# Kernel optimization log

Hardware: AMD Instinct MI355X
Metric: run time of the kernel (lower is better)

Reference implementation:

```python
import jax, jax.numpy as jnp
import numpy as np

D_MODEL = 2048
NHEAD = 32
GROUPS = 8
HEAD_DIM = D_MODEL // NHEAD  # 64
HPG = NHEAD // GROUPS        # heads per group = 4
ROPE_BASE = 10000.0


def _rope(x):
    # x: [B, H, S, D] -- rotate-half RoPE over full head dim, matching RoPE module
    S, D = x.shape[2], x.shape[3]
    theta = 1.0 / (ROPE_BASE ** (jnp.arange(0, D, 2, dtype=jnp.float32) / D))  # [D/2]
    idx_theta = jnp.arange(S, dtype=jnp.float32)[:, None] * theta[None, :]     # [S, D/2]
    ang = jnp.concatenate([idx_theta, idx_theta], axis=-1)                     # [S, D]
    cos = jnp.cos(ang)[None, None]  # [1,1,S,D]
    sin = jnp.sin(ang)[None, None]
    d2 = D // 2
    neg_half = jnp.concatenate([-x[..., d2:], x[..., :d2]], axis=-1)
    return x * cos + neg_half * sin


def setup_inputs() -> dict:
    key = jax.random.key(0)
    ks = jax.random.split(key, 9)
    B, S = 2, 2048
    s_in = 1.0 / np.sqrt(D_MODEL)
    return {
        "x": jax.random.normal(ks[0], (B, S, D_MODEL), jnp.float32),
        "Wq": jax.random.normal(ks[1], (D_MODEL, D_MODEL), jnp.float32) * s_in,
        "bq": jax.random.normal(ks[2], (D_MODEL,), jnp.float32) * 0.01,
        "Wk": jax.random.normal(ks[3], (HEAD_DIM * GROUPS, D_MODEL), jnp.float32) * s_in,
        "bk": jax.random.normal(ks[4], (HEAD_DIM * GROUPS,), jnp.float32) * 0.01,
        "Wv": jax.random.normal(ks[5], (HEAD_DIM * GROUPS, D_MODEL), jnp.float32) * s_in,
        "bv": jax.random.normal(ks[6], (HEAD_DIM * GROUPS,), jnp.float32) * 0.01,
        "Wo": jax.random.normal(ks[7], (D_MODEL, D_MODEL), jnp.float32) * s_in,
        "bo": jax.random.normal(ks[8], (D_MODEL,), jnp.float32) * 0.01,
    }


def reference(x, Wq, bq, Wk, bk, Wv, bv, Wo, bo):
    B, S, _ = x.shape
    # projections (torch Linear: x @ W.T + b)
    q = (x @ Wq.T + bq).reshape(B, S, NHEAD, HEAD_DIM).transpose(0, 2, 1, 3)   # [B,H,S,D]
    k = (x @ Wk.T + bk).reshape(B, S, GROUPS, HEAD_DIM).transpose(0, 2, 1, 3)  # [B,G,S,D]
    v = (x @ Wv.T + bv).reshape(B, S, GROUPS, HEAD_DIM).transpose(0, 2, 1, 3)  # [B,G,S,D]
    q = _rope(q)
    k = _rope(k)
    # grouped-query attention: share each k/v group across HPG query heads
    qg = q.reshape(B, GROUPS, HPG, S, HEAD_DIM)
    scale = 1.0 / np.sqrt(HEAD_DIM)
    scores = jnp.einsum('bghsd,bgtd->bghst', qg, k) * scale  # [B,G,Hpg,S,S]
    causal = jnp.tril(jnp.ones((S, S), dtype=bool))
    scores = jnp.where(causal, scores, jnp.finfo(scores.dtype).min)
    attn = jax.nn.softmax(scores, axis=-1)
    out = jnp.einsum('bghst,bgtd->bghsd', attn, v)           # [B,G,Hpg,S,D]
    out = out.reshape(B, NHEAD, S, HEAD_DIM).transpose(0, 2, 1, 3).reshape(B, S, D_MODEL)
    return out @ Wo.T + bo
```

## Files before the change

kernel.cpp:

```cpp
#include <hip/hip_runtime.h>

typedef unsigned short u16;
typedef __bf16 bf16x8 __attribute__((ext_vector_type(8)));
typedef float floatx4 __attribute__((ext_vector_type(4)));
typedef u16 u16x8 __attribute__((ext_vector_type(8)));
typedef u16 u16x4 __attribute__((ext_vector_type(4)));

#define D_MODEL 2048
#define S_LEN   2048
#define BATCH   2
#define NHEAD   32
#define GROUPS  8
#define HEAD_DIM 64
#define KV_DIM  512
#define KV_LD   1024

__device__ __forceinline__ float bf2f(u16 h) {
  unsigned int u = ((unsigned int)h) << 16;
  return __builtin_bit_cast(float, u);
}
__device__ __forceinline__ u16 f2bf(float f) {
  unsigned int u = __builtin_bit_cast(unsigned int, f);
  u += 0x7fffu + ((u >> 16) & 1u);
  return (u16)(u >> 16);
}
__device__ __forceinline__ float fexp2(float x) {
  float r;
  asm("v_exp_f32 %0, %1" : "=v"(r) : "v"(x));
  return r;
}

#define GLD_LDS(gp, lp) \
  __builtin_amdgcn_global_load_lds((__attribute__((address_space(1))) void*)(gp), \
                                   (__attribute__((address_space(3))) void*)(lp), 16, 0, 0)

__global__ __launch_bounds__(256)
void cvt5_f32_bf16(const float* s0, const float* s1, const float* s2,
                   const float* s3, const float* s4,
                   u16* d0, u16* d1, u16* d2, u16* d3, u16* d4,
                   int n0, int n1, int n2, int n3, int n4)
{
  const float* s; u16* d; int n;
  switch (blockIdx.y) {
    case 0: s = s0; d = d0; n = n0; break;
    case 1: s = s1; d = d1; n = n1; break;
    case 2: s = s2; d = d2; n = n2; break;
    case 3: s = s3; d = d3; n = n3; break;
    default: s = s4; d = d4; n = n4; break;
  }
  long i = ((long)blockIdx.x * 256 + threadIdx.x) * 8;
  if (i >= n) return;
  floatx4 a = *(const floatx4*)(s + i);
  floatx4 b = *(const floatx4*)(s + i + 4);
  u16x8 r;
#pragma unroll
  for (int j = 0; j < 4; ++j) { r[j] = f2bf(a[j]); r[4 + j] = f2bf(b[j]); }
  *(u16x8*)(d + i) = r;
}

template<bool C_F32>
__global__ __launch_bounds__(256, 3)
void gemm_bt_bias(const u16* __restrict__ A, const u16* __restrict__ W,
                  const float* __restrict__ bias, void* __restrict__ Cv,
                  int K, int ldc)
{
  __shared__ __align__(16) u16 As[128 * 32];
  __shared__ __align__(16) u16 Bs[128 * 32];
  const int t = threadIdx.x;
  const int w = t >> 6, l = t & 63;
  const int lr = l & 15, lq = l >> 4;
  const int wm = (w >> 1) * 64, wn = (w & 1) * 64;
  const long bm = (long)blockIdx.x * 128;
  const long bn = (long)blockIdx.y * 128;

  floatx4 acc[4][4] = {};

  const u16* a0 = A + (bm + (t >> 2)) * (long)K + (t & 3) * 8;
  const u16* a1 = a0 + 64L * K;
  const u16* pB0 = W + (bn + (t >> 2)) * (long)K + (t & 3) * 8;
  const u16* pB1 = pB0 + 64L * K;
  u16* As0 = As + w * 512;
  u16* As1 = As + 2048 + w * 512;
  u16* Bs0 = Bs + w * 512;
  u16* Bs1 = Bs + 2048 + w * 512;

  for (int k0 = 0; k0 < K; k0 += 32) {
    GLD_LDS(a0 + k0, As0);
    GLD_LDS(a1 + k0, As1);
    GLD_LDS(pB0 + k0, Bs0);
    GLD_LDS(pB1 + k0, Bs1);
    __syncthreads();

    bf16x8 av[4], bv[4];
#pragma unroll
    for (int i = 0; i < 4; ++i)
      av[i] = *(const bf16x8*)(As + (wm + i * 16 + lr) * 32 + lq * 8);
#pragma unroll
    for (int j = 0; j < 4; ++j)
      bv[j] = *(const bf16x8*)(Bs + (wn + j * 16 + lr) * 32 + lq * 8);
#pragma unroll
    for (int i = 0; i < 4; ++i)
#pragma unroll
      for (int j = 0; j < 4; ++j)
        acc[i][j] = __builtin_amdgcn_mfma_f32_16x16x32_bf16(av[i], bv[j], acc[i][j], 0, 0, 0);
    __syncthreads();
  }

  float bb[4];
#pragma unroll
  for (int j = 0; j < 4; ++j)
    bb[j] = bias[bn + wn + j * 16 + lr];
#pragma unroll
  for (int i = 0; i < 4; ++i) {
#pragma unroll
    for (int rr = 0; rr < 4; ++rr) {
      long row = bm + wm + i * 16 + lq * 4 + rr;
      long cidx = row * (long)ldc + bn + wn + lr;
#pragma unroll
      for (int j = 0; j < 4; ++j) {
        float v = acc[i][j][rr] + bb[j];
        if (C_F32) ((float*)Cv)[cidx + j * 16] = v;
        else       ((u16*)Cv)[cidx + j * 16] = f2bf(v);
      }
    }
  }
}

__global__ __launch_bounds__(256, 3)
void gemm_bt_bias64(const u16* __restrict__ A, const u16* __restrict__ W,
                    const float* __restrict__ bias0, const float* __restrict__ bias1,
                    u16* __restrict__ C, int K, int ldc, int nsplit)
{
  __shared__ __align__(16) u16 As[64 * 32];
  __shared__ __align__(16) u16 Bs[128 * 32];
  const int t = threadIdx.x;
  const int w = t >> 6, l = t & 63;
  const int lr = l & 15, lq = l >> 4;
  const int wm = (w >> 1) * 32, wn = (w & 1) * 64;
  const long bm = (long)blockIdx.x * 64;
  const long bn = (long)blockIdx.y * 128;

  floatx4 acc[2][4] = {};

  const u16* a0 = A + (bm + (t >> 2)) * (long)K + (t & 3) * 8;
  const u16* pB0 = W + (bn + (t >> 2)) * (long)K + (t & 3) * 8;
  const u16* pB1 = pB0 + 64L * K;
  u16* As0 = As + w * 512;
  u16* Bs0 = Bs + w * 512;
  u16* Bs1 = Bs + 2048 + w * 512;

  for (int k0 = 0; k0 < K; k0 += 32) {
    GLD_LDS(a0 + k0, As0);
    GLD_LDS(pB0 + k0, Bs0);
    GLD_LDS(pB1 + k0, Bs1);
    __syncthreads();

    bf16x8 av[2], bv[4];
#pragma unroll
    for (int i = 0; i < 2; ++i)
      av[i] = *(const bf16x8*)(As + (wm + i * 16 + lr) * 32 + lq * 8);
#pragma unroll
    for (int j = 0; j < 4; ++j)
      bv[j] = *(const bf16x8*)(Bs + (wn + j * 16 + lr) * 32 + lq * 8);
#pragma unroll
    for (int i = 0; i < 2; ++i)
#pragma unroll
      for (int j = 0; j < 4; ++j)
        acc[i][j] = __builtin_amdgcn_mfma_f32_16x16x32_bf16(av[i], bv[j], acc[i][j], 0, 0, 0);
    __syncthreads();
  }

  const float* bias = (bn < nsplit) ? bias0 : (bias1 - nsplit);
  float bb[4];
#pragma unroll
  for (int j = 0; j < 4; ++j)
    bb[j] = bias[bn + wn + j * 16 + lr];
#pragma unroll
  for (int i = 0; i < 2; ++i) {
#pragma unroll
    for (int rr = 0; rr < 4; ++rr) {
      long row = bm + wm + i * 16 + lq * 4 + rr;
      long cidx = row * (long)ldc + bn + wn + lr;
#pragma unroll
      for (int j = 0; j < 4; ++j)
        C[cidx + j * 16] = f2bf(acc[i][j][rr] + bb[j]);
    }
  }
}

__global__ __launch_bounds__(256)
void rope_kernel(u16* __restrict__ Q, u16* __restrict__ KV)
{
  const int bs = blockIdx.x;
  const int s = bs & (S_LEN - 1);
  const int t = threadIdx.x;
  u16* qrow = Q + (long)bs * D_MODEL;
#pragma unroll
  for (int i = 0; i < 4; ++i) {
    int p = t + i * 256;
    int hh = p >> 5, d = p & 31;
    float theta = __expf(-(float)d * 0.28782313662425574f);
    float sn, cs;
    sincosf((float)s * theta, &sn, &cs);
    int i0 = hh * 64 + d;
    float x0 = bf2f(qrow[i0]), x1 = bf2f(qrow[i0 + 32]);
    qrow[i0]      = f2bf(x0 * cs - x1 * sn);
    qrow[i0 + 32] = f2bf(x1 * cs + x0 * sn);
  }
  u16* krow = KV + (long)bs * KV_LD;
  {
    int g = t >> 5, d = t & 31;
    float theta = __expf(-(float)d * 0.28782313662425574f);
    float sn, cs;
    sincosf((float)s * theta, &sn, &cs);
    int i0 = g * 64 + d;
    float x0 = bf2f(krow[i0]), x1 = bf2f(krow[i0 + 32]);
    krow[i0]      = f2bf(x0 * cs - x1 * sn);
    krow[i0 + 32] = f2bf(x1 * cs + x0 * sn);
  }
}

__global__ __launch_bounds__(256)
void vtrans(const u16* __restrict__ KV, u16* __restrict__ Vt)
{
  __shared__ __align__(16) u16 tile[64][72];
  const int ts = blockIdx.x * 64;
  const int tc = blockIdx.y * 64;
  const int b  = blockIdx.z;
  const int t  = threadIdx.x;
#pragma unroll
  for (int i = 0; i < 2; ++i) {
    int c = t + i * 256;
    int r = c >> 3, c8 = (c & 7) * 8;
    u16x8 v = *(const u16x8*)(KV + ((long)b * S_LEN + ts + r) * KV_LD + 512 + tc + c8);
    *(u16x8*)&tile[r][c8] = v;
  }
  __syncthreads();
#pragma unroll
  for (int i = 0; i < 2; ++i) {
    int c = t + i * 256;
    int r = c >> 3, c8 = (c & 7) * 8;
    u16x8 v;
#pragma unroll
    for (int e = 0; e < 8; ++e) v[e] = tile[c8 + e][r];
    *(u16x8*)(Vt + ((long)b * KV_DIM + tc + r) * S_LEN + ts + c8) = v;
  }
}

__global__ __launch_bounds__(256, 3)
void gqa_attn(const u16* Q, const u16* __restrict__ Kc,
              const u16* __restrict__ Vt, u16* O)
{
  __shared__ __align__(16) u16 KV[2][16 * 512];
  __shared__ __align__(16) u16 Ps[4][2][16 * 72];

  const int pr = blockIdx.x;
  const int bh = blockIdx.y;
  const int b = bh >> 5, h = bh & 31, g = h >> 2;

  const int t = threadIdx.x;
  const int w = t >> 6, l = t & 63;
  const int lr = l & 15, lq = l >> 4;

  const u16* Kp = Kc + ((long)b * S_LEN) * KV_LD + g * HEAD_DIM;
  const u16* Vp = Vt + ((long)b * KV_DIM + g * HEAD_DIM) * S_LEN;

  long sb[4];
  {
    const int sig2 = ((l >> 2) ^ (l >> 4)) & 1;
    const int sig1 = ((l >> 1) ^ (l >> 3)) & 1;
    const int sig0 = (l ^ sig2) & 1;
    const int row = ((l >> 2) & 14) | sig2;
    const int cl = ((sig1 << 1) | sig0) * 8;
#pragma unroll
    for (int q = 0; q < 4; ++q) {
      const int r = (w & 1) * 4 + q;
      const int jj = r >> 1, cc = r & 1;
      sb[q] = (w < 2) ? ((long)(jj * 16 + row) * KV_LD + cc * 32 + cl)
                      : ((long)(jj * 16 + row) * S_LEN + cc * 32 + cl);
    }
  }
  const u16* sp = (w < 2) ? Kp : Vp;
  const long smul = (w < 2) ? (long)64 * KV_LD : 64;
  const int dbase = ((w < 2) ? 0 : 4096) + (w & 1) * 2048;
  const int koff = ((4 * lr + lq) ^ (lr & 7)) * 8;

#define STAGE(bufi, kt_) do { \
    const long soff_ = (long)(kt_) * smul; \
    GLD_LDS(sp + soff_ + sb[0], &KV[bufi][dbase + 0 * 512]); \
    GLD_LDS(sp + soff_ + sb[1], &KV[bufi][dbase + 1 * 512]); \
    GLD_LDS(sp + soff_ + sb[2], &KV[bufi][dbase + 2 * 512]); \
    GLD_LDS(sp + soff_ + sb[3], &KV[bufi][dbase + 3 * 512]); \
  } while (0)

#define TILE(ktv, D0, D1) do { \
    const u16* buf_ = &KV[(ktv) & 1][0]; \
    floatx4 z0[4] = {}, z1[4] = {}; \
    _Pragma("unroll") \
    for (int j = 0; j < 4; ++j) { \
      bf16x8 kf0 = *(const bf16x8*)(buf_ + j * 1024 + koff); \
      bf16x8 kf1 = *(const bf16x8*)(buf_ + j * 1024 + 512 + koff); \
      if (!(D1) && (!(D0) || j <= w)) { \
        z0[j] = __builtin_amdgcn_mfma_f32_16x16x32_bf16(kf0, qf00, z0[j], 0, 0, 0); \
        z0[j] = __builtin_amdgcn_mfma_f32_16x16x32_bf16(kf1, qf01, z0[j], 0, 0, 0); \
      } \
      if (!(D1) || j <= w) { \
        z1[j] = __builtin_amdgcn_mfma_f32_16x16x32_bf16(kf0, qf10, z1[j], 0, 0, 0); \
        z1[j] = __builtin_amdgcn_mfma_f32_16x16x32_bf16(kf1, qf11, z1[j], 0, 0, 0); \
      } \
    } \
    if (!(D1)) { \
      _Pragma("unroll") \
      for (int j = 0; j < 4; ++j) { \
        u16x4 pk; \
        _Pragma("unroll") \
        for (int rr = 0; rr < 4; ++rr) { \
          float ps; \
          if ((D0) && (j * 16 + lq * 4 + rr > w * 16 + lr)) ps = 0.f; \
          else ps = fexp2(z0[j][rr] * 0.18033688011112042f - 23.083120654223414f); \
          ls0 += ps; \
          pk[rr] = __builtin_bit_cast(u16, (__bf16)ps); \
        } \
        *(u16x4*)&Ps[w][0][lr * 72 + j * 16 + lq * 4] = pk; \
      } \
    } \
    _Pragma("unroll") \
    for (int j = 0; j < 4; ++j) { \
      u16x4 pk; \
      _Pragma("unroll") \
      for (int rr = 0; rr < 4; ++rr) { \
        float ps; \
        if ((D1) && (j * 16 + lq * 4 + rr > w * 16 + lr)) ps = 0.f; \
        else ps = fexp2(z1[j][rr] * 0.18033688011112042f - 23.083120654223414f); \
        ls1 += ps; \
        pk[rr] = __builtin_bit_cast(u16, (__bf16)ps); \
      } \
      *(u16x4*)&Ps[w][1][lr * 72 + j * 16 + lq * 4] = pk; \
    } \
    bf16x8 pa00 = *(const bf16x8*)&Ps[w][0][lr * 72 + lq * 8]; \
    bf16x8 pa01 = *(const bf16x8*)&Ps[w][0][lr * 72 + 32 + lq * 8]; \
    bf16x8 pa10 = *(const bf16x8*)&Ps[w][1][lr * 72 + lq * 8]; \
    bf16x8 pa11 = *(const bf16x8*)&Ps[w][1][lr * 72 + 32 + lq * 8]; \
    const u16* vbuf_ = buf_ + 4096; \
    _Pragma("unroll") \
    for (int j = 0; j < 4; ++j) { \
      bf16x8 vb0 = *(const bf16x8*)(vbuf_ + j * 1024 + koff); \
      bf16x8 vb1 = *(const bf16x8*)(vbuf_ + j * 1024 + 512 + koff); \
      if (!(D1)) { \
        o0[j] = __builtin_amdgcn_mfma_f32_16x16x32_bf16(pa00, vb0, o0[j], 0, 0, 0); \
        if (!(D0) || w >= 2) \
          o0[j] = __builtin_amdgcn_mfma_f32_16x16x32_bf16(pa01, vb1, o0[j], 0, 0, 0); \
      } \
      o1[j] = __builtin_amdgcn_mfma_f32_16x16x32_bf16(pa10, vb0, o1[j], 0, 0, 0); \
      if (!(D1) || w >= 2) \
        o1[j] = __builtin_amdgcn_mfma_f32_16x16x32_bf16(pa11, vb1, o1[j], 0, 0, 0); \
    } \
  } while (0)

#pragma unroll 1
  for (int seg = 0; seg < 2; ++seg) {
    const int qt = seg ? (15 - pr) : pr;
    const u16* Qp = Q + ((long)b * S_LEN + qt * 128) * D_MODEL + h * HEAD_DIM;
    u16* Op = O + ((long)b * S_LEN + qt * 128) * D_MODEL + h * HEAD_DIM;

    bf16x8 qf00, qf01, qf10, qf11;
    {
      const u16* qr0 = Qp + (long)(w * 16 + lr) * D_MODEL;
      qf00 = *(const bf16x8*)(qr0 + lq * 8);
      qf01 = *(const bf16x8*)(qr0 + 32 + lq * 8);
      const u16* qr1 = qr0 + (long)64 * D_MODEL;
      qf10 = *(const bf16x8*)(qr1 + lq * 8);
      qf11 = *(const bf16x8*)(qr1 + 32 + lq * 8);
    }

    floatx4 o0[4] = {}, o1[4] = {};
    float ls0 = 0.f, ls1 = 0.f;
    const int NKT = 2 * qt + 2;

    if (seg) __syncthreads();
    STAGE(0, 0);
    for (int kt = 0; kt < NKT - 2; ++kt) {
      __syncthreads();
      STAGE((kt + 1) & 1, kt + 1);
      TILE(kt, false, false);
    }
    __syncthreads();
    STAGE((NKT - 1) & 1, NKT - 1);
    TILE(NKT - 2, true, false);
    __syncthreads();
    TILE(NKT - 1, false, true);

#pragma unroll
    for (int s = 0; s < 2; ++s) {
      float ls = s ? ls1 : ls0;
      ls += __shfl_xor(ls, 16);
      ls += __shfl_xor(ls, 32);
      const floatx4* oo = s ? o1 : o0;
#pragma unroll
      for (int rr = 0; rr < 4; ++rr) {
        float lrow = __shfl(ls, lq * 4 + rr);
        float inv = 1.f / lrow;
        long row = s * 64 + w * 16 + lq * 4 + rr;
        u16* op = Op + row * (long)D_MODEL + lr;
#pragma unroll
        for (int j = 0; j < 4; ++j)
          op[j * 16] = f2bf(oo[j][rr] * inv);
      }
    }
  }
#undef TILE
#undef STAGE
}

extern "C" void kernel_launch(void* const* d_in, const int* in_sizes, int n_in,
                              void* d_out, int out_size, void* d_ws, size_t ws_size,
                              hipStream_t stream)
{
  const float* x  = (const float*)d_in[0];
  const float* Wq = (const float*)d_in[1];
  const float* bq = (const float*)d_in[2];
  const float* Wk = (const float*)d_in[3];
  const float* bk = (const float*)d_in[4];
  const float* Wv = (const float*)d_in[5];
  const float* bv = (const float*)d_in[6];
  const float* Wo = (const float*)d_in[7];
  const float* bo = (const float*)d_in[8];
  float* out = (float*)d_out;

  const int Sx  = BATCH * S_LEN * D_MODEL;
  const int SWq = D_MODEL * D_MODEL;
  const int SWk = KV_DIM * D_MODEL;
  const int SWv = KV_DIM * D_MODEL;
  const int SWo = D_MODEL * D_MODEL;

  u16* xb  = (u16*)d_ws;
  u16* Wqb = xb  + Sx;
  u16* Wkb = Wqb + SWq;
  u16* Wvb = Wkb + SWk;
  u16* Wob = Wvb + SWv;
  u16* Qb  = Wob + SWo;
  u16* KVb = Qb + (size_t)4096 * 2048;
  u16* Vtb = KVb + (size_t)4096 * 1024;
  u16* AO  = Qb;

  const int M = BATCH * S_LEN;
  dim3 blk(256);
  cvt5_f32_bf16<<<dim3(4096, 5), blk, 0, stream>>>(x, Wq, Wk, Wv, Wo,
                                                   xb, Wqb, Wkb, Wvb, Wob,
                                                   Sx, SWq, SWk, SWv, SWo);
  gemm_bt_bias<false><<<dim3(M / 128, D_MODEL / 128), blk, 0, stream>>>(xb, Wqb, bq, Qb, D_MODEL, D_MODEL);
  gemm_bt_bias64<<<dim3(M / 64, KV_LD / 128), blk, 0, stream>>>(xb, Wkb, bk, bv, KVb, D_MODEL, KV_LD, KV_DIM);
  vtrans<<<dim3(S_LEN / 64, KV_DIM / 64, BATCH), blk, 0, stream>>>(KVb, Vtb);
  rope_kernel<<<dim3(M), blk, 0, stream>>>(Qb, KVb);
  gqa_attn<<<dim3(8, BATCH * NHEAD), blk, 0, stream>>>(Qb, KVb, Vtb, AO);
  gemm_bt_bias<true><<<dim3(M / 128, D_MODEL / 128), blk, 0, stream>>>(AO, Wob, bo, out, D_MODEL, D_MODEL);
}
```

Measured before the change: 320.9 us.

## Fuse RoPE and V transpose into projection GEMM epilogues with precomputed tables

Builds cos/sin RoPE tables inside the conversion kernel and applies rotation directly in the Q and K GEMM epilogues, where each lane holds both halves of a head. The V projection epilogue writes a transposed V buffer directly. This removes the separate rope and vtrans kernels and their global round trips. K moves to its own compact buffer. The cost is extra table loads in the epilogues and scattered 4-element stores for the transposed V.

```diff
diff --git a/kernel.cpp b/kernel.cpp
--- a/kernel.cpp
+++ b/kernel.cpp
@@ -13,7 +13,6 @@
 #define GROUPS  8
 #define HEAD_DIM 64
 #define KV_DIM  512
-#define KV_LD   1024
 
 __device__ __forceinline__ float bf2f(u16 h) {
   unsigned int u = ((unsigned int)h) << 16;
@@ -38,8 +37,20 @@
 void cvt5_f32_bf16(const float* s0, const float* s1, const float* s2,
                    const float* s3, const float* s4,
                    u16* d0, u16* d1, u16* d2, u16* d3, u16* d4,
-                   int n0, int n1, int n2, int n3, int n4)
+                   int n0, int n1, int n2, int n3, int n4,
+                   float* ct, float* st)
 {
+  if (blockIdx.y == 5) {
+    int idx = blockIdx.x * 256 + threadIdx.x;
+    if (idx < S_LEN * 32) {
+      int s = idx >> 5, d = idx & 31;
+      float theta = __expf(-(float)d * 0.28782313662425574f);
+      float sn, cs;
+      sincosf((float)s * theta, &sn, &cs);
+      ct[idx] = cs; st[idx] = sn;
+    }
+    return;
+  }
   const float* s; u16* d; int n;
   switch (blockIdx.y) {
     case 0: s = s0; d = d0; n = n0; break;
@@ -58,10 +69,11 @@
   *(u16x8*)(d + i) = r;
 }
 
-template<bool C_F32>
+template<int MODE>
 __global__ __launch_bounds__(256, 3)
 void gemm_bt_bias(const u16* __restrict__ A, const u16* __restrict__ W,
                   const float* __restrict__ bias, void* __restrict__ Cv,
+                  const float* __restrict__ ct, const float* __restrict__ st,
                   int K, int ldc)
 {
   __shared__ __align__(16) u16 As[128 * 32];
@@ -110,26 +122,41 @@
 #pragma unroll
   for (int j = 0; j < 4; ++j)
     bb[j] = bias[bn + wn + j * 16 + lr];
+
 #pragma unroll
   for (int i = 0; i < 4; ++i) {
 #pragma unroll
     for (int rr = 0; rr < 4; ++rr) {
       long row = bm + wm + i * 16 + lq * 4 + rr;
       long cidx = row * (long)ldc + bn + wn + lr;
-#pragma unroll
-      for (int j = 0; j < 4; ++j) {
-        float v = acc[i][j][rr] + bb[j];
-        if (C_F32) ((float*)Cv)[cidx + j * 16] = v;
-        else       ((u16*)Cv)[cidx + j * 16] = f2bf(v);
+      if (MODE == 1) {
+        float* cp = (float*)Cv + cidx;
+#pragma unroll
+        for (int j = 0; j < 4; ++j)
+          cp[j * 16] = acc[i][j][rr] + bb[j];
+      } else {
+        int srow = (int)row & (S_LEN - 1);
+        float c0 = ct[srow * 32 + lr],      sn0 = st[srow * 32 + lr];
+        float c1 = ct[srow * 32 + 16 + lr], sn1 = st[srow * 32 + 16 + lr];
+        float v0 = acc[i][0][rr] + bb[0];
+        float v1 = acc[i][1][rr] + bb[1];
+        float v2 = acc[i][2][rr] + bb[2];
+        float v3 = acc[i][3][rr] + bb[3];
+        u16* cp = (u16*)Cv + cidx;
+        cp[0]  = f2bf(v0 * c0 - v2 * sn0);
+        cp[16] = f2bf(v1 * c1 - v3 * sn1);
+        cp[32] = f2bf(v2 * c0 + v0 * sn0);
+        cp[48] = f2bf(v3 * c1 + v1 * sn1);
       }
     }
   }
 }
 
 __global__ __launch_bounds__(256, 3)
-void gemm_bt_bias64(const u16* __restrict__ A, const u16* __restrict__ W,
-                    const float* __restrict__ bias0, const float* __restrict__ bias1,
-                    u16* __restrict__ C, int K, int ldc, int nsplit)
+void gemm_kv(const u16* __restrict__ A, const u16* __restrict__ W,
+             const float* __restrict__ bkb, const float* __restrict__ bvb,
+             u16* __restrict__ Kb, u16* __restrict__ Vt,
+             const float* __restrict__ ct, const float* __restrict__ st, int K)
 {
   __shared__ __align__(16) u16 As[64 * 32];
   __shared__ __align__(16) u16 Bs[128 * 32];
@@ -155,95 +182,64 @@
     GLD_LDS(pB1 + k0, Bs1);
     __syncthreads();
 
-    bf16x8 av[2], bv[4];
+    bf16x8 av[2], bv8[4];
 #pragma unroll
     for (int i = 0; i < 2; ++i)
       av[i] = *(const bf16x8*)(As + (wm + i * 16 + lr) * 32 + lq * 8);
 #pragma unroll
     for (int j = 0; j < 4; ++j)
-      bv[j] = *(const bf16x8*)(Bs + (wn + j * 16 + lr) * 32 + lq * 8);
+      bv8[j] = *(const bf16x8*)(Bs + (wn + j * 16 + lr) * 32 + lq * 8);
 #pragma unroll
     for (int i = 0; i < 2; ++i)
 #pragma unroll
       for (int j = 0; j < 4; ++j)
-        acc[i][j] = __builtin_amdgcn_mfma_f32_16x16x32_bf16(av[i], bv[j], acc[i][j], 0, 0, 0);
-    __syncthreads();
-  }
-
-  const float* bias = (bn < nsplit) ? bias0 : (bias1 - nsplit);
-  float bb[4];
-#pragma unroll
-  for (int j = 0; j < 4; ++j)
-    bb[j] = bias[bn + wn + j * 16 + lr];
-#pragma unroll
-  for (int i = 0; i < 2; ++i) {
-#pragma unroll
-    for (int rr = 0; rr < 4; ++rr) {
-      long row = bm + wm + i * 16 + lq * 4 + rr;
-      long cidx = row * (long)ldc + bn + wn + lr;
-#pragma unroll
-      for (int j = 0; j < 4; ++j)
-        C[cidx + j * 16] = f2bf(acc[i][j][rr] + bb[j]);
-    }
-  }
-}
-
-__global__ __launch_bounds__(256)
-void rope_kernel(u16* __restrict__ Q, u16* __restrict__ KV)
-{
-  const int bs = blockIdx.x;
-  const int s = bs & (S_LEN - 1);
-  const int t = threadIdx.x;
-  u16* qrow = Q + (long)bs * D_MODEL;
-#pragma unroll
-  for (int i = 0; i < 4; ++i) {
-    int p = t + i * 256;
-    int hh = p >> 5, d = p & 31;
-    float theta = __expf(-(float)d * 0.28782313662425574f);
-    float sn, cs;
-    sincosf((float)s * theta, &sn, &cs);
-    int i0 = hh * 64 + d;
-    float x0 = bf2f(qrow[i0]), x1 = bf2f(qrow[i0 + 32]);
-    qrow[i0]      = f2bf(x0 * cs - x1 * sn);
-    qrow[i0 + 32] = f2bf(x1 * cs + x0 * sn);
-  }
-  u16* krow = KV + (long)bs * KV_LD;
-  {
-    int g = t >> 5, d = t & 31;
-    float theta = __expf(-(float)d * 0.28782313662425574f);
-    float sn, cs;
-    sincosf((float)s * theta, &sn, &cs);
-    int i0 = g * 64 + d;
-    float x0 = bf2f(krow[i0]), x1 = bf2f(krow[i0 + 32]);
-    krow[i0]      = f2bf(x0 * cs - x1 * sn);
-    krow[i0 + 32] = f2bf(x1 * cs + x0 * sn);
-  }
-}
-
-__global__ __launch_bounds__(256)
-void vtrans(const u16* __restrict__ KV, u16* __restrict__ Vt)
-{
-  __shared__ __align__(16) u16 tile[64][72];
-  const int ts = blockIdx.x * 64;
-  const int tc = blockIdx.y * 64;
-  const int b  = blockIdx.z;
-  const int t  = threadIdx.x;
-#pragma unroll
-  for (int i = 0; i < 2; ++i) {
-    int c = t + i * 256;
-    int r = c >> 3, c8 = (c & 7) * 8;
-    u16x8 v = *(const u16x8*)(KV + ((long)b * S_LEN + ts + r) * KV_LD + 512 + tc + c8);
-    *(u16x8*)&tile[r][c8] = v;
-  }
-  __syncthreads();
-#pragma unroll
-  for (int i = 0; i < 2; ++i) {
-    int c = t + i * 256;
-    int r = c >> 3, c8 = (c & 7) * 8;
-    u16x8 v;
-#pragma unroll
-    for (int e = 0; e < 8; ++e) v[e] = tile[c8 + e][r];
-    *(u16x8*)(Vt + ((long)b * KV_DIM + tc + r) * S_LEN + ts + c8) = v;
+        acc[i][j] = __builtin_amdgcn_mfma_f32_16x16x32_bf16(av[i], bv8[j], acc[i][j], 0, 0, 0);
+    __syncthreads();
+  }
+
+  if (bn < KV_DIM) {
+    float bb[4];
+#pragma unroll
+    for (int j = 0; j < 4; ++j)
+      bb[j] = bkb[bn + wn + j * 16 + lr];
+#pragma unroll
+    for (int i = 0; i < 2; ++i) {
+#pragma unroll
+      for (int rr = 0; rr < 4; ++rr) {
+        long row = bm + wm + i * 16 + lq * 4 + rr;
+        int srow = (int)row & (S_LEN - 1);
+        float c0 = ct[srow * 32 + lr],      sn0 = st[srow * 32 + lr];
+        float c1 = ct[srow * 32 + 16 + lr], sn1 = st[srow * 32 + 16 + lr];
+        float v0 = acc[i][0][rr] + bb[0];
+        float v1 = acc[i][1][rr] + bb[1];
+        float v2 = acc[i][2][rr] + bb[2];
+        float v3 = acc[i][3][rr] + bb[3];
+        u16* cp = Kb + row * (long)KV_DIM + bn + wn + lr;
+        cp[0]  = f2bf(v0 * c0 - v2 * sn0);
+        cp[16] = f2bf(v1 * c1 - v3 * sn1);
+        cp[32] = f2bf(v2 * c0 + v0 * sn0);
+        cp[48] = f2bf(v3 * c1 + v1 * sn1);
+      }
+    }
+  } else {
+    float bb[4];
+#pragma unroll
+    for (int j = 0; j < 4; ++j)
+      bb[j] = bvb[bn - KV_DIM + wn + j * 16 + lr];
+#pragma unroll
+    for (int i = 0; i < 2; ++i) {
+      int row0 = (int)bm + wm + i * 16 + lq * 4;
+      int b = row0 >> 11, s0r = row0 & (S_LEN - 1);
+#pragma unroll
+      for (int j = 0; j < 4; ++j) {
+        int vcol = (int)bn - KV_DIM + wn + j * 16 + lr;
+        u16x4 pv;
+#pragma unroll
+        for (int rr = 0; rr < 4; ++rr)
+          pv[rr] = f2bf(acc[i][j][rr] + bb[j]);
+        *(u16x4*)(Vt + ((long)b * KV_DIM + vcol) * S_LEN + s0r) = pv;
+      }
+    }
   }
 }
 
@@ -262,7 +258,7 @@
   const int w = t >> 6, l = t & 63;
   const int lr = l & 15, lq = l >> 4;
 
-  const u16* Kp = Kc + ((long)b * S_LEN) * KV_LD + g * HEAD_DIM;
+  const u16* Kp = Kc + ((long)b * S_LEN) * KV_DIM + g * HEAD_DIM;
   const u16* Vp = Vt + ((long)b * KV_DIM + g * HEAD_DIM) * S_LEN;
 
   long sb[4];
@@ -276,12 +272,12 @@
     for (int q = 0; q < 4; ++q) {
       const int r = (w & 1) * 4 + q;
       const int jj = r >> 1, cc = r & 1;
-      sb[q] = (w < 2) ? ((long)(jj * 16 + row) * KV_LD + cc * 32 + cl)
+      sb[q] = (w < 2) ? ((long)(jj * 16 + row) * KV_DIM + cc * 32 + cl)
                       : ((long)(jj * 16 + row) * S_LEN + cc * 32 + cl);
     }
   }
   const u16* sp = (w < 2) ? Kp : Vp;
-  const long smul = (w < 2) ? (long)64 * KV_LD : 64;
+  const long smul = (w < 2) ? (long)64 * KV_DIM : 64;
   const int dbase = ((w < 2) ? 0 : 4096) + (w & 1) * 2048;
   const int koff = ((4 * lr + lq) ^ (lr & 7)) * 8;
 
@@ -439,19 +435,20 @@
   u16* Wvb = Wkb + SWk;
   u16* Wob = Wvb + SWv;
   u16* Qb  = Wob + SWo;
-  u16* KVb = Qb + (size_t)4096 * 2048;
-  u16* Vtb = KVb + (size_t)4096 * 1024;
+  u16* Kb  = Qb + (size_t)4096 * 2048;
+  u16* Vtb = Kb + (size_t)4096 * 512;
+  float* ctab = (float*)(Vtb + (size_t)BATCH * KV_DIM * S_LEN);
+  float* stab = ctab + S_LEN * 32;
   u16* AO  = Qb;
 
   const int M = BATCH * S_LEN;
   dim3 blk(256);
-  cvt5_f32_bf16<<<dim3(4096, 5), blk, 0, stream>>>(x, Wq, Wk, Wv, Wo,
+  cvt5_f32_bf16<<<dim3(4096, 6), blk, 0, stream>>>(x, Wq, Wk, Wv, Wo,
                                                    xb, Wqb, Wkb, Wvb, Wob,
-                                                   Sx, SWq, SWk, SWv, SWo);
-  gemm_bt_bias<false><<<dim3(M / 128, D_MODEL / 128), blk, 0, stream>>>(xb, Wqb, bq, Qb, D_MODEL, D_MODEL);
-  gemm_bt_bias64<<<dim3(M / 64, KV_LD / 128), blk, 0, stream>>>(xb, Wkb, bk, bv, KVb, D_MODEL, KV_LD, KV_DIM);
-  vtrans<<<dim3(S_LEN / 64, KV_DIM / 64, BATCH), blk, 0, stream>>>(KVb, Vtb);
-  rope_kernel<<<dim3(M), blk, 0, stream>>>(Qb, KVb);
-  gqa_attn<<<dim3(8, BATCH * NHEAD), blk, 0, stream>>>(Qb, KVb, Vtb, AO);
-  gemm_bt_bias<true><<<dim3(M / 128, D_MODEL / 128), blk, 0, stream>>>(AO, Wob, bo, out, D_MODEL, D_MODEL);
-}
+                                                   Sx, SWq, SWk, SWv, SWo,
+                                                   ctab, stab);
+  gemm_bt_bias<2><<<dim3(M / 128, D_MODEL / 128), blk, 0, stream>>>(xb, Wqb, bq, Qb, ctab, stab, D_MODEL, D_MODEL);
+  gemm_kv<<<dim3(M / 64, 1024 / 128), blk, 0, stream>>>(xb, Wkb, bk, bv, Kb, Vtb, ctab, stab, D_MODEL);
+  gqa_attn<<<dim3(8, BATCH * NHEAD), blk, 0, stream>>>(Qb, Kb, Vtb, AO);
+  gemm_bt_bias<1><<<dim3(M / 128, D_MODEL / 128), blk, 0, stream>>>(AO, Wob, bo, out, ctab, stab, D_MODEL, D_MODEL);
+}
```

Result: faster. 310.8 us (-3.2%).
